# Performance work log

Hardware: AMD Instinct MI355X
Metric: run time of the kernel (lower is better)

## Reference

```python
import math
import jax, jax.numpy as jnp
import numpy as np

V, D, A, H, FF, L, MD = 500, 512, 512, 8, 2048, 6, 512
HD = A // H
B, S, T = 32, 512, 128


def setup_inputs() -> dict:
    key = jax.random.key(0)
    ks = jax.random.split(key, 40)
    init = lambda k, shape: (jax.random.normal(k, shape, jnp.float32) * 0.02)
    inp = {
        'memory': jax.random.normal(ks[0], (B, S, MD), jnp.float32),
        'memory_lens': jax.random.randint(ks[1], (B,), S // 2, S + 1),
        'ys_in_pad': jax.random.randint(ks[2], (B, T), 0, V),
        'ys_in_lens': jax.random.randint(ks[3], (B,), T // 2, T + 1),
        'emb': init(ks[4], (V, D)),
        'w_out': init(ks[5], (D, V)),
        'b_out': jnp.zeros((V,), jnp.float32),
        # per-layer params stacked on leading L axis (consumed by lax.scan)
        'ln_sa_g': jnp.ones((L, D), jnp.float32), 'ln_sa_b': jnp.zeros((L, D), jnp.float32),
        'sa_wq': init(ks[6], (L, D, A)), 'sa_bq': init(ks[7], (L, A)),
        'sa_wk': init(ks[8], (L, D, A)), 'sa_bk': init(ks[9], (L, A)),
        'sa_wv': init(ks[10], (L, D, A)), 'sa_bv': init(ks[11], (L, A)),
        'sa_wo': init(ks[12], (L, A, D)), 'sa_bo': init(ks[13], (L, D)),
        'ln_ca_g': jnp.ones((L, D), jnp.float32), 'ln_ca_b': jnp.zeros((L, D), jnp.float32),
        'ca_wq': init(ks[14], (L, D, A)), 'ca_bq': init(ks[15], (L, A)),
        'ca_wk': init(ks[16], (L, MD, A)), 'ca_bk': init(ks[17], (L, A)),
        'ca_wv': init(ks[18], (L, MD, A)), 'ca_bv': init(ks[19], (L, A)),
        'ca_wo': init(ks[20], (L, A, D)), 'ca_bo': init(ks[21], (L, D)),
        'ln_ff_g': jnp.ones((L, D), jnp.float32), 'ln_ff_b': jnp.zeros((L, D), jnp.float32),
        'ff_w1': init(ks[22], (L, D, FF)), 'ff_b1': init(ks[23], (L, FF)),
        'ff_w2': init(ks[24], (L, FF, D)), 'ff_b2': init(ks[25], (L, D)),
    }
    return inp


def _layernorm(x, g, b, eps=1e-5):
    m = jnp.mean(x, axis=-1, keepdims=True)
    v = jnp.mean(jnp.square(x - m), axis=-1, keepdims=True)
    return (x - m) * jax.lax.rsqrt(v + eps) * g + b


def _mha(q_in, k_in, v_in, mask, wq, bq, wk, bk, wv, bv, wo, bo):
    # mask: True = disallowed. (B, T, S) for self-attn, (B, 1, S) for cross-attn.
    b_, tq, _ = q_in.shape
    ts = k_in.shape[1]
    q = (q_in @ wq + bq).reshape(b_, tq, H, HD).transpose(0, 2, 1, 3)
    k = (k_in @ wk + bk).reshape(b_, ts, H, HD).transpose(0, 2, 1, 3)
    v = (v_in @ wv + bv).reshape(b_, ts, H, HD).transpose(0, 2, 1, 3)
    s = jnp.einsum('bhtd,bhsd->bhts', q, k) / math.sqrt(HD)
    # penalize_abs_values_gt(limit=50, penalty=1e-4) is identity in the forward
    # pass (it only injects an auxiliary gradient during training).
    s = jnp.where(mask[:, None, :, :], -jnp.inf, s)
    a = jax.nn.softmax(s, axis=-1)  # dropout p=0.0 in this config
    o = jnp.einsum('bhts,bhsd->bhtd', a, v).transpose(0, 2, 1, 3).reshape(b_, tq, A)
    return o @ wo + bo


def _forward(memory, memory_lens, ys_in_pad, ys_in_lens, emb, w_out, b_out, layer_params):
    t = ys_in_pad.shape[1]
    # make_pad_mask | ~subsequent_mask  -> (B, T, T), True = masked
    pad = jnp.arange(t)[None, :] >= ys_in_lens[:, None]            # (B, T)
    causal = ~jnp.tril(jnp.ones((t, t), bool))                     # (T, T)
    tgt_mask = pad[:, None, :] | causal[None]                      # (B, T, T)
    mem_mask = (jnp.arange(memory.shape[1])[None, :] >= memory_lens[:, None])[:, None, :]

    # embedding + sinusoidal positional encoding (dropout in eval = identity)
    pos = jnp.arange(t, dtype=jnp.float32)[:, None]
    div = jnp.exp(jnp.arange(0, D, 2, dtype=jnp.float32) * (-math.log(10000.0) / D))
    pe = jnp.zeros((t, D), jnp.float32)
    pe = pe.at[:, 0::2].set(jnp.sin(pos * div)).at[:, 1::2].set(jnp.cos(pos * div))
    x = emb[ys_in_pad] * math.sqrt(D) + pe[None]

    def step(tgt, p):
        tn = _layernorm(tgt, p['ln_sa_g'], p['ln_sa_b'])
        tgt = tgt + _mha(tn, tn, tn, tgt_mask,
                         p['sa_wq'], p['sa_bq'], p['sa_wk'], p['sa_bk'],
                         p['sa_wv'], p['sa_bv'], p['sa_wo'], p['sa_bo'])
        tn = _layernorm(tgt, p['ln_ca_g'], p['ln_ca_b'])
        tgt = tgt + _mha(tn, memory, memory, mem_mask,
                         p['ca_wq'], p['ca_bq'], p['ca_wk'], p['ca_bk'],
                         p['ca_wv'], p['ca_bv'], p['ca_wo'], p['ca_bo'])
        tn = _layernorm(tgt, p['ln_ff_g'], p['ln_ff_b'])
        h = tn @ p['ff_w1'] + p['ff_b1']
        h = h * jax.nn.sigmoid(h)  # Swish
        tgt = tgt + h @ p['ff_w2'] + p['ff_b2']
        return tgt, None

    x, _ = jax.lax.scan(step, x, layer_params)
    return x @ w_out + b_out  # (B, T, V) logits


_LAYER_KEYS = ['ln_sa_g', 'ln_sa_b', 'sa_wq', 'sa_bq', 'sa_wk', 'sa_bk', 'sa_wv', 'sa_bv',
               'sa_wo', 'sa_bo', 'ln_ca_g', 'ln_ca_b', 'ca_wq', 'ca_bq', 'ca_wk', 'ca_bk',
               'ca_wv', 'ca_bv', 'ca_wo', 'ca_bo', 'ln_ff_g', 'ln_ff_b',
               'ff_w1', 'ff_b1', 'ff_w2', 'ff_b2']


def reference(memory, memory_lens, ys_in_pad, ys_in_lens, emb, w_out, b_out,
              ln_sa_g, ln_sa_b, sa_wq, sa_bq, sa_wk, sa_bk, sa_wv, sa_bv, sa_wo, sa_bo,
              ln_ca_g, ln_ca_b, ca_wq, ca_bq, ca_wk, ca_bk, ca_wv, ca_bv, ca_wo, ca_bo,
              ln_ff_g, ln_ff_b, ff_w1, ff_b1, ff_w2, ff_b2):
    loc = locals()
    layer_params = {k: loc[k] for k in _LAYER_KEYS}
    return _forward(memory, memory_lens, ys_in_pad, ys_in_lens, emb, w_out, b_out, layer_params)
```

## Files before the change

### kernel.cpp

```cpp
#include <hip/hip_runtime.h>
#include <hip/hip_bf16.h>
#include <hip/hip_fp16.h>

constexpr int Bc = 32, Sc = 512, Tc = 128, Dc = 512, Ac = 512, Hc = 8;
constexpr int HDc = 64, FFc = 2048, Lc = 6, Vc = 500;
constexpr int NTOK = Bc * Tc;
constexpr int NMEM = Bc * Sc;

typedef unsigned short u16;
typedef __attribute__((ext_vector_type(8))) short short8;
typedef __attribute__((ext_vector_type(4))) float f32x4;

__device__ __forceinline__ u16 bfc(float x) {
  __hip_bfloat16 h = __float2bfloat16(x);
  return *reinterpret_cast<u16*>(&h);
}

__device__ __forceinline__ void gload16(const void* g, void* l) {
  __builtin_amdgcn_global_load_lds(
      (const __attribute__((address_space(1))) unsigned int*)g,
      (__attribute__((address_space(3))) unsigned int*)l, 16, 0, 0);
}

__device__ __forceinline__ float wave_sum(float v) {
#pragma unroll
  for (int o = 32; o > 0; o >>= 1) v += __shfl_down(v, o);
  return v;
}
__device__ __forceinline__ float wave_max(float v) {
#pragma unroll
  for (int o = 32; o > 0; o >>= 1) v = fmaxf(v, __shfl_down(v, o));
  return v;
}

__global__ __launch_bounds__(256) void embed_pe_k(const int* __restrict__ ys,
                                                  const float* __restrict__ emb,
                                                  float* __restrict__ x) {
  int tok = blockIdx.x;
  int t = tok & (Tc - 1);
  int id = ys[tok];
  int j = threadIdx.x;
  int d0 = 2 * j;
  const float cdiv = -9.210340371976184f / (float)Dc;
  float div = expf((float)d0 * cdiv);
  float ang = (float)t * div;
  float pe0 = sinf(ang), pe1 = cosf(ang);
  const float sc = 22.627416997969522f;
  long base = (long)tok * Dc + d0;
  long ebase = (long)id * Dc + d0;
  x[base]     = emb[ebase]     * sc + pe0;
  x[base + 1] = emb[ebase + 1] * sc + pe1;
}

__global__ __launch_bounds__(256) void layernorm_k(const float* __restrict__ x,
                                                   const float* __restrict__ g,
                                                   const float* __restrict__ bta,
                                                   u16* __restrict__ out) {
  int row = blockIdx.x;
  int tid = threadIdx.x;
  const float* xr = x + (long)row * Dc;
  float2 xv = *(const float2*)(xr + tid * 2);
  __shared__ float red[4];
  float s = wave_sum(xv.x + xv.y);
  if ((tid & 63) == 0) red[tid >> 6] = s;
  __syncthreads();
  float mean = (red[0] + red[1] + red[2] + red[3]) * (1.0f / Dc);
  float dx0 = xv.x - mean, dx1 = xv.y - mean;
  __syncthreads();
  float s2 = wave_sum(dx0 * dx0 + dx1 * dx1);
  if ((tid & 63) == 0) red[tid >> 6] = s2;
  __syncthreads();
  float var = (red[0] + red[1] + red[2] + red[3]) * (1.0f / Dc);
  float rstd = rsqrtf(var + 1e-5f);
  ushort2 o;
  o.x = bfc(dx0 * rstd * g[2 * tid] + bta[2 * tid]);
  o.y = bfc(dx1 * rstd * g[2 * tid + 1] + bta[2 * tid + 1]);
  *(ushort2*)(out + (long)row * Dc + tid * 2) = o;
}

__global__ __launch_bounds__(256) void wtrans_k(const float* __restrict__ src,
                                                u16* __restrict__ dst,
                                                int K, int N, long srcStride, long dstStride) {
  int z = blockIdx.z;
  src += z * srcStride;
  dst += z * dstStride;
  __shared__ float t[32][33];
  int n0 = blockIdx.x * 32, k0 = blockIdx.y * 32;
  int tx = threadIdx.x & 31, ty = threadIdx.x >> 5;
#pragma unroll
  for (int i = 0; i < 4; i++) {
    int n = n0 + tx;
    t[ty + 8 * i][tx] = (n < N) ? src[(long)(k0 + ty + 8 * i) * N + n] : 0.0f;
  }
  __syncthreads();
#pragma unroll
  for (int i = 0; i < 4; i++) {
    dst[(long)(n0 + ty + 8 * i) * K + k0 + tx] = bfc(t[tx][ty + 8 * i]);
  }
}

__global__ __launch_bounds__(256) void vtrans_k(const u16* __restrict__ V,
                                                u16* __restrict__ Vt, int Scur) {
  int b = blockIdx.z;
  int c0 = blockIdx.x * 32, s0 = blockIdx.y * 32;
  __shared__ u16 t[32][33];
  int tx = threadIdx.x & 31, ty = threadIdx.x >> 5;
#pragma unroll
  for (int i = 0; i < 4; i++)
    t[ty + 8 * i][tx] = V[((long)b * Scur + s0 + ty + 8 * i) * 512 + c0 + tx];
  __syncthreads();
#pragma unroll
  for (int i = 0; i < 4; i++)
    Vt[((long)b * 512 + c0 + ty + 8 * i) * Scur + s0 + tx] = t[tx][ty + 8 * i];
}

__global__ __launch_bounds__(256) void f2b_k(const float* __restrict__ in,
                                             u16* __restrict__ out, long n) {
  long i = ((long)blockIdx.x * 256 + threadIdx.x) * 4;
  if (i >= n) return;
  float4 v = *(const float4*)(in + i);
  ushort4 o;
  o.x = bfc(v.x); o.y = bfc(v.y); o.z = bfc(v.z); o.w = bfc(v.w);
  *(ushort4*)(out + i) = o;
}

template <int BMW, int OMODE, bool BIAS, bool RES, bool SWISH, bool NCH>
__global__ __launch_bounds__(256) void mgemm_k(
    const u16* __restrict__ A, const u16* __restrict__ Bt,
    const float* __restrict__ bias0, const float* __restrict__ bias1,
    const float* __restrict__ bias2,
    void* __restrict__ Cv, const float* __restrict__ R,
    int N, int K, int lda, int ldb, int ldc, int nbi,
    long batAo, long batAi, long batBo, long batBi, long batCo, long batCi) {
  constexpr int BM = BMW * 32;
  int z = blockIdx.z;
  int bo = z / nbi, bi = z - bo * nbi;
  const u16* Ab = A + bo * batAo + bi * batAi;
  const u16* Bb = Bt + bo * batBo + bi * batBi;
  long coff = bo * batCo + bi * batCi;
  const float* bias = nullptr;
  if constexpr (BIAS) bias = (bi == 0) ? bias0 : ((bi == 1) ? bias1 : bias2);
  int m0 = blockIdx.y * BM, n0 = blockIdx.x * 128;

  __shared__ __align__(16) u16 As[BM * 32];
  __shared__ __align__(16) u16 Bs[128 * 32];

  int tid = threadIdx.x;
  int lane = tid & 63, wid = tid >> 6;
  int wm = wid >> 1, wn = wid & 1;
  int fr = lane & 15, grp = lane >> 4;

  f32x4 acc[BMW][4];
#pragma unroll
  for (int i = 0; i < BMW; i++)
#pragma unroll
    for (int j = 0; j < 4; j++) acc[i][j] = (f32x4){0.f, 0.f, 0.f, 0.f};

  const u16* ga = Ab + (long)(m0 + (tid >> 2)) * lda + ((tid & 3) << 3);
  const u16* gb = Bb + (long)(n0 + (tid >> 2)) * ldb + ((tid & 3) << 3);
  u16* lA = &As[tid * 8];
  u16* lB = &Bs[tid * 8];

  for (int kt = 0; kt < K; kt += 32) {
    gload16(ga + kt, lA);
    if constexpr (BM == 128) gload16(ga + kt + (long)64 * lda, lA + 2048);
    gload16(gb + kt, lB);
    gload16(gb + kt + (long)64 * ldb, lB + 2048);
    __syncthreads();
    short8 av[BMW], bv[4];
#pragma unroll
    for (int i = 0; i < BMW; i++)
      av[i] = *(const short8*)&As[(wm * BMW * 16 + i * 16 + fr) * 32 + grp * 8];
#pragma unroll
    for (int j = 0; j < 4; j++)
      bv[j] = *(const short8*)&Bs[(wn * 64 + j * 16 + fr) * 32 + grp * 8];
#pragma unroll
    for (int i = 0; i < BMW; i++)
#pragma unroll
      for (int j = 0; j < 4; j++)
        acc[i][j] = __builtin_amdgcn_mfma_f32_16x16x32_bf16(av[i], bv[j], acc[i][j], 0, 0, 0);
    __syncthreads();
  }

  int rbase = m0 + wm * BMW * 16 + grp * 4;
  int cbase = n0 + wn * 64 + fr;
#pragma unroll
  for (int i = 0; i < BMW; i++) {
#pragma unroll
    for (int j = 0; j < 4; j++) {
      int col = cbase + j * 16;
      if (NCH && col >= N) continue;
      float bb = 0.0f;
      if constexpr (BIAS) bb = bias[col];
#pragma unroll
      for (int r = 0; r < 4; r++) {
        int row = rbase + i * 16 + r;
        float v = acc[i][j][r] + bb;
        long idx = coff + (long)row * ldc + col;
        if constexpr (RES) v += R[idx];
        if constexpr (SWISH) v = v / (1.0f + expf(-v));
        if constexpr (OMODE == 0) ((u16*)Cv)[idx] = bfc(v);
        else ((float*)Cv)[idx] = v;
      }
    }
  }
}

template <int SKV, int KVBLK, bool CAUSAL>
__global__ __launch_bounds__(256) void fattn_k(
    const u16* __restrict__ Q, const u16* __restrict__ Kg, const u16* __restrict__ Vtg,
    u16* __restrict__ O, const int* __restrict__ lens) {
  constexpr int NJ  = KVBLK / 16;
  constexpr int NKV = KVBLK / 32;
  constexpr int NT  = SKV / KVBLK;
  constexpr int KST = 72;
  constexpr int VST = KVBLK + 8;
  constexpr int CHK = KVBLK * 8 / 256;
  constexpr int CHV = 64 * (KVBLK / 8) / 256;

  __shared__ __align__(16) u16 Ks[KVBLK * KST];
  __shared__ __align__(16) u16 Vs[64 * VST];
  __shared__ __align__(16) u16 Ps[128 * VST];

  int bh = blockIdx.x; int b = bh >> 3, h = bh & 7;
  int tid = threadIdx.x, lane = tid & 63, wid = tid >> 6;
  int fr = lane & 15, grp = lane >> 4;
  int len = lens[b];

  short8 qa[2][2];
  {
    const u16* qp = Q + ((long)b * Tc + wid * 32 + fr) * 512 + h * 64 + grp * 8;
#pragma unroll
    for (int i = 0; i < 2; i++)
#pragma unroll
      for (int k2 = 0; k2 < 2; k2++)
        qa[i][k2] = *(const short8*)(qp + (long)i * 16 * 512 + k2 * 32);
  }

  float m_run[2][4], l_run[2][4];
  f32x4 acc_o[2][4];
#pragma unroll
  for (int i = 0; i < 2; i++)
#pragma unroll
    for (int r = 0; r < 4; r++) { m_run[i][r] = -1e30f; l_run[i][r] = 0.0f; }
#pragma unroll
  for (int i = 0; i < 2; i++)
#pragma unroll
    for (int j = 0; j < 4; j++) acc_o[i][j] = (f32x4){0.f, 0.f, 0.f, 0.f};

  const u16* Kbase = Kg + ((long)b * SKV) * 512 + h * 64;
  const u16* Vbase = Vtg + ((long)b * 512 + h * 64) * SKV;

  short8 kreg[CHK], vreg[CHV];
#pragma unroll
  for (int c = 0; c < CHK; c++) {
    int idx = tid + 256 * c; int kv = idx >> 3, s = idx & 7;
    kreg[c] = *(const short8*)(Kbase + (long)kv * 512 + s * 8);
  }
#pragma unroll
  for (int c = 0; c < CHV; c++) {
    int idx = tid + 256 * c; int d = idx / (KVBLK / 8), sk = idx % (KVBLK / 8);
    vreg[c] = *(const short8*)(Vbase + (long)d * SKV + sk * 8);
  }

  for (int t = 0; t < NT; t++) {
    int kv0 = t * KVBLK;
    __syncthreads();
#pragma unroll
    for (int c = 0; c < CHK; c++) {
      int idx = tid + 256 * c; int kv = idx >> 3, s = idx & 7;
      *(short8*)&Ks[kv * KST + s * 8] = kreg[c];
    }
#pragma unroll
    for (int c = 0; c < CHV; c++) {
      int idx = tid + 256 * c; int d = idx / (KVBLK / 8), sk = idx % (KVBLK / 8);
      *(short8*)&Vs[d * VST + sk * 8] = vreg[c];
    }
    __syncthreads();
    if (t + 1 < NT) {
      int kvn = kv0 + KVBLK;
#pragma unroll
      for (int c = 0; c < CHK; c++) {
        int idx = tid + 256 * c; int kv = idx >> 3, s = idx & 7;
        kreg[c] = *(const short8*)(Kbase + (long)(kvn + kv) * 512 + s * 8);
      }
#pragma unroll
      for (int c = 0; c < CHV; c++) {
        int idx = tid + 256 * c; int d = idx / (KVBLK / 8), sk = idx % (KVBLK / 8);
        vreg[c] = *(const short8*)(Vbase + (long)d * SKV + kvn + sk * 8);
      }
    }

    int jmax = NJ;
    if constexpr (CAUSAL) jmax = (wid * 32 + 31 - kv0) / 16 + 1;

    f32x4 accs[2][NJ];
#pragma unroll
    for (int j = 0; j < NJ; j++) {
      if (CAUSAL && j >= jmax) continue;
      short8 bv0 = *(const short8*)&Ks[(j * 16 + fr) * KST + grp * 8];
      short8 bv1 = *(const short8*)&Ks[(j * 16 + fr) * KST + 32 + grp * 8];
#pragma unroll
      for (int i = 0; i < 2; i++) {
        f32x4 a = __builtin_amdgcn_mfma_f32_16x16x32_bf16(qa[i][0], bv0, (f32x4){0.f,0.f,0.f,0.f}, 0, 0, 0);
        accs[i][j] = __builtin_amdgcn_mfma_f32_16x16x32_bf16(qa[i][1], bv1, a, 0, 0, 0);
      }
    }

    float alpha[2][4];
#pragma unroll
    for (int i = 0; i < 2; i++) {
#pragma unroll
      for (int r = 0; r < 4; r++) {
        int qrow = wid * 32 + i * 16 + grp * 4 + r;
        float vmax = -1e30f;
#pragma unroll
        for (int j = 0; j < NJ; j++) {
          if (CAUSAL && j >= jmax) continue;
          int kvb = kv0 + j * 16 + fr;
          float s = accs[i][j][r] * 0.125f;
          bool msk = (kvb >= len) || (CAUSAL && kvb > qrow);
          s = msk ? -1e30f : s;
          accs[i][j][r] = s;
          vmax = fmaxf(vmax, s);
        }
        vmax = fmaxf(vmax, __shfl_xor(vmax, 1));
        vmax = fmaxf(vmax, __shfl_xor(vmax, 2));
        vmax = fmaxf(vmax, __shfl_xor(vmax, 4));
        vmax = fmaxf(vmax, __shfl_xor(vmax, 8));
        float mn = fmaxf(m_run[i][r], vmax);
        float al = __expf(m_run[i][r] - mn);
        m_run[i][r] = mn;
        alpha[i][r] = al;
        float rs = 0.0f;
#pragma unroll
        for (int j = 0; j < NJ; j++) {
          if (CAUSAL && j >= jmax) continue;
          float p = __expf(accs[i][j][r] - mn);
          accs[i][j][r] = p;
          rs += p;
        }
        rs += __shfl_xor(rs, 1);
        rs += __shfl_xor(rs, 2);
        rs += __shfl_xor(rs, 4);
        rs += __shfl_xor(rs, 8);
        l_run[i][r] = l_run[i][r] * al + rs;
      }
    }

#pragma unroll
    for (int i = 0; i < 2; i++)
#pragma unroll
      for (int j = 0; j < NJ; j++) {
        if (CAUSAL && j >= jmax) continue;
#pragma unroll
        for (int r = 0; r < 4; r++) {
          int prow = wid * 32 + i * 16 + grp * 4 + r;
          Ps[prow * VST + j * 16 + fr] = bfc(accs[i][j][r]);
        }
      }

#pragma unroll
    for (int i = 0; i < 2; i++)
#pragma unroll
      for (int jd = 0; jd < 4; jd++)
#pragma unroll
        for (int r = 0; r < 4; r++)
          acc_o[i][jd][r] *= alpha[i][r];

    int kvmax = NKV;
    if constexpr (CAUSAL) kvmax = wid + 1;
#pragma unroll
    for (int kk = 0; kk < NKV; kk++) {
      if (CAUSAL && kk >= kvmax) continue;
      short8 pa[2];
#pragma unroll
      for (int i = 0; i < 2; i++)
        pa[i] = *(const short8*)&Ps[(wid * 32 + i * 16 + fr) * VST + kk * 32 + grp * 8];
#pragma unroll
      for (int jd = 0; jd < 4; jd++) {
        short8 vb = *(const short8*)&Vs[(jd * 16 + fr) * VST + kk * 32 + grp * 8];
#pragma unroll
        for (int i = 0; i < 2; i++)
          acc_o[i][jd] = __builtin_amdgcn_mfma_f32_16x16x32_bf16(pa[i], vb, acc_o[i][jd], 0, 0, 0);
      }
    }
  }

#pragma unroll
  for (int i = 0; i < 2; i++) {
#pragma unroll
    for (int r = 0; r < 4; r++) {
      float inv = 1.0f / l_run[i][r];
      long tok = (long)b * Tc + wid * 32 + i * 16 + grp * 4 + r;
#pragma unroll
      for (int jd = 0; jd < 4; jd++)
        O[tok * 512 + h * 64 + jd * 16 + fr] = bfc(acc_o[i][jd][r] * inv);
    }
  }
}

extern "C" void kernel_launch(void* const* d_in, const int* in_sizes, int n_in,
                              void* d_out, int out_size, void* d_ws, size_t ws_size,
                              hipStream_t stream) {
  const float* memory   = (const float*)d_in[0];
  const int*   mem_lens = (const int*)d_in[1];
  const int*   ys       = (const int*)d_in[2];
  const int*   ys_lens  = (const int*)d_in[3];
  const float* emb      = (const float*)d_in[4];
  const float* w_out    = (const float*)d_in[5];
  const float* b_out    = (const float*)d_in[6];
  const float* pp[26];
  for (int i = 0; i < 26; i++) pp[i] = (const float*)d_in[7 + i];

  constexpr long PLW = 4194304;
  constexpr long OFF_SAQ = 0, OFF_SAK = 262144, OFF_SAV = 524288, OFF_SAO = 786432,
                 OFF_CAQ = 1048576, OFF_CAK = 1310720, OFF_CAV = 1572864,
                 OFF_CAO = 1835008, OFF_FF1 = 2097152, OFF_FF2 = 3145728,
                 OFF_WOUT = 6 * PLW;
  u16*   Wt   = (u16*)d_ws;
  float* X    = (float*)(Wt + 25427968);
  u16*   TO   = (u16*)(X + 2097152);
  u16*   QKV  = TO + 2097152;
  u16*   memb = QKV + 3 * 2097152;
  u16*   Kb   = memb + 8388608;
  u16*   SCw  = Kb + 8388608;
  u16*   Vt   = SCw + 16777216;
  float* OUT  = (float*)d_out;

  auto WT = [&](const float* src, long dstoff, int K, int N, int Npad, int Lz,
                long srcStride, long dstStride) {
    dim3 g(Npad / 32, K / 32, Lz);
    wtrans_k<<<g, 256, 0, stream>>>(src, Wt + dstoff, K, N, srcStride, dstStride);
  };
  WT(pp[2],  OFF_SAQ, 512, 512, 512, Lc, 262144, PLW);
  WT(pp[4],  OFF_SAK, 512, 512, 512, Lc, 262144, PLW);
  WT(pp[6],  OFF_SAV, 512, 512, 512, Lc, 262144, PLW);
  WT(pp[8],  OFF_SAO, 512, 512, 512, Lc, 262144, PLW);
  WT(pp[12], OFF_CAQ, 512, 512, 512, Lc, 262144, PLW);
  WT(pp[14], OFF_CAK, 512, 512, 512, Lc, 262144, PLW);
  WT(pp[16], OFF_CAV, 512, 512, 512, Lc, 262144, PLW);
  WT(pp[18], OFF_CAO, 512, 512, 512, Lc, 262144, PLW);
  WT(pp[22], OFF_FF1, 512, 2048, 2048, Lc, 1048576, PLW);
  WT(pp[24], OFF_FF2, 2048, 512, 512, Lc, 1048576, PLW);
  WT(w_out,  OFF_WOUT, 512, 500, 512, 1, 0, 0);

  f2b_k<<<(NMEM * Dc / 4 + 255) / 256, 256, 0, stream>>>(memory, memb, (long)NMEM * Dc);
  embed_pe_k<<<NTOK, 256, 0, stream>>>(ys, emb, X);

  for (int l = 0; l < Lc; l++) {
    const u16* WtL = Wt + (long)l * PLW;

    layernorm_k<<<NTOK, 256, 0, stream>>>(X, pp[0] + (long)l * Dc, pp[1] + (long)l * Dc, TO);
    mgemm_k<2, 0, true, false, false, false><<<dim3(4, 64, 3), 256, 0, stream>>>(
        TO, WtL + OFF_SAQ, pp[3] + (long)l * Ac, pp[5] + (long)l * Ac, pp[7] + (long)l * Ac,
        QKV, nullptr, 512, 512, 512, 512, 512, 3, 0, 0, 0, 262144, 0, 2097152);
    vtrans_k<<<dim3(16, 4, Bc), 256, 0, stream>>>(QKV + 2 * 2097152, Vt, Tc);
    fattn_k<128, 128, true><<<256, 256, 0, stream>>>(
        QKV, QKV + 2097152, Vt, TO, ys_lens);
    mgemm_k<2, 1, true, true, false, false><<<dim3(4, 64, 1), 256, 0, stream>>>(
        TO, WtL + OFF_SAO, pp[9] + (long)l * Dc, nullptr, nullptr, X, X,
        512, 512, 512, 512, 512, 1, 0, 0, 0, 0, 0, 0);

    layernorm_k<<<NTOK, 256, 0, stream>>>(X, pp[10] + (long)l * Dc, pp[11] + (long)l * Dc, TO);
    mgemm_k<2, 0, true, false, false, false><<<dim3(4, 64, 1), 256, 0, stream>>>(
        TO, WtL + OFF_CAQ, pp[13] + (long)l * Ac, nullptr, nullptr, QKV, nullptr,
        512, 512, 512, 512, 512, 1, 0, 0, 0, 0, 0, 0);
    mgemm_k<4, 0, true, false, false, false><<<dim3(4, 128, 2), 256, 0, stream>>>(
        memb, WtL + OFF_CAK, pp[15] + (long)l * Ac, pp[17] + (long)l * Ac, nullptr,
        Kb, nullptr, 512, 512, 512, 512, 512, 2, 0, 0, 0, 262144, 0, 8388608);
    vtrans_k<<<dim3(16, 16, Bc), 256, 0, stream>>>(SCw, Vt, Sc);
    fattn_k<512, 64, false><<<256, 256, 0, stream>>>(
        QKV, Kb, Vt, TO, mem_lens);
    mgemm_k<2, 1, true, true, false, false><<<dim3(4, 64, 1), 256, 0, stream>>>(
        TO, WtL + OFF_CAO, pp[19] + (long)l * Dc, nullptr, nullptr, X, X,
        512, 512, 512, 512, 512, 1, 0, 0, 0, 0, 0, 0);

    layernorm_k<<<NTOK, 256, 0, stream>>>(X, pp[20] + (long)l * Dc, pp[21] + (long)l * Dc, TO);
    mgemm_k<2, 0, true, false, true, false><<<dim3(16, 64, 1), 256, 0, stream>>>(
        TO, WtL + OFF_FF1, pp[23] + (long)l * FFc, nullptr, nullptr, SCw, nullptr,
        2048, 512, 512, 512, 2048, 1, 0, 0, 0, 0, 0, 0);
    mgemm_k<2, 1, true, true, false, false><<<dim3(4, 64, 1), 256, 0, stream>>>(
        SCw, WtL + OFF_FF2, pp[25] + (long)l * Dc, nullptr, nullptr, X, X,
        512, 2048, 2048, 2048, 512, 1, 0, 0, 0, 0, 0, 0);
  }

  f2b_k<<<(NTOK * Dc / 4 + 255) / 256, 256, 0, stream>>>(X, TO, (long)NTOK * Dc);
  mgemm_k<2, 1, true, false, false, true><<<dim3(4, 64, 1), 256, 0, stream>>>(
      TO, Wt + OFF_WOUT, b_out, nullptr, nullptr, OUT, nullptr,
      500, 512, 512, 512, 500, 1, 0, 0, 0, 0, 0, 0);
}
```

Baseline: 1.305 ms.

## Double-buffer GEMM LDS, drop V transpose, add attention row-split and tile skipping

The GEMM kernel now double-buffers its shared-memory tiles so the next K-slice loads while the current one is multiplied. The separate V-transpose kernels are removed, and the attention kernel transposes V into shared memory itself with scalar stores. It also skips KV tiles past the causal limit or the sequence length, and splits query rows across blocks for cross-attention. Larger BM tiles are used for the QKV and FF1 GEMMs. The scalar transposed LDS stores may cause bank conflicts, and doubling LDS can reduce occupancy.

```diff
diff --git a/kernel.cpp b/kernel.cpp
--- a/kernel.cpp
+++ b/kernel.cpp
@@ -99,21 +99,6 @@
   }
 }
 
-__global__ __launch_bounds__(256) void vtrans_k(const u16* __restrict__ V,
-                                                u16* __restrict__ Vt, int Scur) {
-  int b = blockIdx.z;
-  int c0 = blockIdx.x * 32, s0 = blockIdx.y * 32;
-  __shared__ u16 t[32][33];
-  int tx = threadIdx.x & 31, ty = threadIdx.x >> 5;
-#pragma unroll
-  for (int i = 0; i < 4; i++)
-    t[ty + 8 * i][tx] = V[((long)b * Scur + s0 + ty + 8 * i) * 512 + c0 + tx];
-  __syncthreads();
-#pragma unroll
-  for (int i = 0; i < 4; i++)
-    Vt[((long)b * 512 + c0 + ty + 8 * i) * Scur + s0 + tx] = t[tx][ty + 8 * i];
-}
-
 __global__ __launch_bounds__(256) void f2b_k(const float* __restrict__ in,
                                              u16* __restrict__ out, long n) {
   long i = ((long)blockIdx.x * 256 + threadIdx.x) * 4;
@@ -142,8 +127,8 @@
   if constexpr (BIAS) bias = (bi == 0) ? bias0 : ((bi == 1) ? bias1 : bias2);
   int m0 = blockIdx.y * BM, n0 = blockIdx.x * 128;
 
-  __shared__ __align__(16) u16 As[BM * 32];
-  __shared__ __align__(16) u16 Bs[128 * 32];
+  __shared__ __align__(16) u16 As[2][BM * 32];
+  __shared__ __align__(16) u16 Bs[2][128 * 32];
 
   int tid = threadIdx.x;
   int lane = tid & 63, wid = tid >> 6;
@@ -158,29 +143,41 @@
 
   const u16* ga = Ab + (long)(m0 + (tid >> 2)) * lda + ((tid & 3) << 3);
   const u16* gb = Bb + (long)(n0 + (tid >> 2)) * ldb + ((tid & 3) << 3);
-  u16* lA = &As[tid * 8];
-  u16* lB = &Bs[tid * 8];
-
-  for (int kt = 0; kt < K; kt += 32) {
+
+  auto STAGE = [&](int buf, int kt) {
+    u16* lA = &As[buf][tid * 8];
+    u16* lB = &Bs[buf][tid * 8];
     gload16(ga + kt, lA);
     if constexpr (BM == 128) gload16(ga + kt + (long)64 * lda, lA + 2048);
     gload16(gb + kt, lB);
     gload16(gb + kt + (long)64 * ldb, lB + 2048);
-    __syncthreads();
+  };
+
+  auto COMPUTE = [&](int buf) {
     short8 av[BMW], bv[4];
 #pragma unroll
     for (int i = 0; i < BMW; i++)
-      av[i] = *(const short8*)&As[(wm * BMW * 16 + i * 16 + fr) * 32 + grp * 8];
+      av[i] = *(const short8*)&As[buf][(wm * BMW * 16 + i * 16 + fr) * 32 + grp * 8];
 #pragma unroll
     for (int j = 0; j < 4; j++)
-      bv[j] = *(const short8*)&Bs[(wn * 64 + j * 16 + fr) * 32 + grp * 8];
+      bv[j] = *(const short8*)&Bs[buf][(wn * 64 + j * 16 + fr) * 32 + grp * 8];
 #pragma unroll
     for (int i = 0; i < BMW; i++)
 #pragma unroll
       for (int j = 0; j < 4; j++)
         acc[i][j] = __builtin_amdgcn_mfma_f32_16x16x32_bf16(av[i], bv[j], acc[i][j], 0, 0, 0);
+  };
+
+  STAGE(0, 0);
+  __syncthreads();
+  int cur = 0;
+  for (int kt = 32; kt < K; kt += 32) {
+    STAGE(cur ^ 1, kt);
+    COMPUTE(cur);
     __syncthreads();
-  }
+    cur ^= 1;
+  }
+  COMPUTE(cur);
 
   int rbase = m0 + wm * BMW * 16 + grp * 4;
   int cbase = n0 + wn * 64 + fr;
@@ -206,113 +203,114 @@
   }
 }
 
-template <int SKV, int KVBLK, bool CAUSAL>
+template <int SKV, int KVBLK, bool CAUSAL, int IQ>
 __global__ __launch_bounds__(256) void fattn_k(
-    const u16* __restrict__ Q, const u16* __restrict__ Kg, const u16* __restrict__ Vtg,
+    const u16* __restrict__ Q, const u16* __restrict__ Kg, const u16* __restrict__ Vg,
     u16* __restrict__ O, const int* __restrict__ lens) {
   constexpr int NJ  = KVBLK / 16;
   constexpr int NKV = KVBLK / 32;
   constexpr int NT  = SKV / KVBLK;
   constexpr int KST = 72;
   constexpr int VST = KVBLK + 8;
-  constexpr int CHK = KVBLK * 8 / 256;
-  constexpr int CHV = 64 * (KVBLK / 8) / 256;
+  constexpr int WR  = 16 * IQ;
+  constexpr int WGR = 64 * IQ;
+  constexpr int CH  = KVBLK / 32;
 
   __shared__ __align__(16) u16 Ks[KVBLK * KST];
   __shared__ __align__(16) u16 Vs[64 * VST];
-  __shared__ __align__(16) u16 Ps[128 * VST];
+  __shared__ __align__(16) u16 Ps[WGR * VST];
 
   int bh = blockIdx.x; int b = bh >> 3, h = bh & 7;
+  int row00 = blockIdx.y * WGR;
   int tid = threadIdx.x, lane = tid & 63, wid = tid >> 6;
   int fr = lane & 15, grp = lane >> 4;
   int len = lens[b];
-
-  short8 qa[2][2];
+  int row0w = row00 + wid * WR;
+
+  short8 qa[IQ][2];
   {
-    const u16* qp = Q + ((long)b * Tc + wid * 32 + fr) * 512 + h * 64 + grp * 8;
-#pragma unroll
-    for (int i = 0; i < 2; i++)
+    const u16* qp = Q + ((long)b * Tc + row0w + fr) * 512 + h * 64 + grp * 8;
+#pragma unroll
+    for (int i = 0; i < IQ; i++)
 #pragma unroll
       for (int k2 = 0; k2 < 2; k2++)
         qa[i][k2] = *(const short8*)(qp + (long)i * 16 * 512 + k2 * 32);
   }
 
-  float m_run[2][4], l_run[2][4];
-  f32x4 acc_o[2][4];
-#pragma unroll
-  for (int i = 0; i < 2; i++)
+  float m_run[IQ][4], l_run[IQ][4];
+  f32x4 acc_o[IQ][4];
+#pragma unroll
+  for (int i = 0; i < IQ; i++)
 #pragma unroll
     for (int r = 0; r < 4; r++) { m_run[i][r] = -1e30f; l_run[i][r] = 0.0f; }
 #pragma unroll
-  for (int i = 0; i < 2; i++)
+  for (int i = 0; i < IQ; i++)
 #pragma unroll
     for (int j = 0; j < 4; j++) acc_o[i][j] = (f32x4){0.f, 0.f, 0.f, 0.f};
 
   const u16* Kbase = Kg + ((long)b * SKV) * 512 + h * 64;
-  const u16* Vbase = Vtg + ((long)b * 512 + h * 64) * SKV;
-
-  short8 kreg[CHK], vreg[CHV];
-#pragma unroll
-  for (int c = 0; c < CHK; c++) {
+  const u16* Vbase = Vg + ((long)b * SKV) * 512 + h * 64;
+
+  int NTeff = NT;
+  if constexpr (CAUSAL) NTeff = (row00 + WGR - 1) / KVBLK + 1;
+  int lenT = (len + KVBLK - 1) / KVBLK;
+  if (lenT < NTeff) NTeff = lenT;
+
+  short8 kreg[CH], vreg[CH];
+#pragma unroll
+  for (int c = 0; c < CH; c++) {
     int idx = tid + 256 * c; int kv = idx >> 3, s = idx & 7;
     kreg[c] = *(const short8*)(Kbase + (long)kv * 512 + s * 8);
-  }
-#pragma unroll
-  for (int c = 0; c < CHV; c++) {
-    int idx = tid + 256 * c; int d = idx / (KVBLK / 8), sk = idx % (KVBLK / 8);
-    vreg[c] = *(const short8*)(Vbase + (long)d * SKV + sk * 8);
-  }
-
-  for (int t = 0; t < NT; t++) {
+    vreg[c] = *(const short8*)(Vbase + (long)kv * 512 + s * 8);
+  }
+
+  for (int t = 0; t < NTeff; t++) {
     int kv0 = t * KVBLK;
     __syncthreads();
 #pragma unroll
-    for (int c = 0; c < CHK; c++) {
+    for (int c = 0; c < CH; c++) {
       int idx = tid + 256 * c; int kv = idx >> 3, s = idx & 7;
       *(short8*)&Ks[kv * KST + s * 8] = kreg[c];
-    }
-#pragma unroll
-    for (int c = 0; c < CHV; c++) {
-      int idx = tid + 256 * c; int d = idx / (KVBLK / 8), sk = idx % (KVBLK / 8);
-      *(short8*)&Vs[d * VST + sk * 8] = vreg[c];
+#pragma unroll
+      for (int j = 0; j < 8; j++)
+        Vs[(s * 8 + j) * VST + kv] = (u16)vreg[c][j];
     }
     __syncthreads();
-    if (t + 1 < NT) {
+    if (t + 1 < NTeff) {
       int kvn = kv0 + KVBLK;
 #pragma unroll
-      for (int c = 0; c < CHK; c++) {
+      for (int c = 0; c < CH; c++) {
         int idx = tid + 256 * c; int kv = idx >> 3, s = idx & 7;
         kreg[c] = *(const short8*)(Kbase + (long)(kvn + kv) * 512 + s * 8);
-      }
-#pragma unroll
-      for (int c = 0; c < CHV; c++) {
-        int idx = tid + 256 * c; int d = idx / (KVBLK / 8), sk = idx % (KVBLK / 8);
-        vreg[c] = *(const short8*)(Vbase + (long)d * SKV + kvn + sk * 8);
+        vreg[c] = *(const short8*)(Vbase + (long)(kvn + kv) * 512 + s * 8);
       }
     }
 
     int jmax = NJ;
-    if constexpr (CAUSAL) jmax = (wid * 32 + 31 - kv0) / 16 + 1;
-
-    f32x4 accs[2][NJ];
+    if constexpr (CAUSAL) {
+      jmax = (row0w + WR - 1 - kv0) / 16 + 1;
+      if (jmax > NJ) jmax = NJ;
+    }
+
+    f32x4 accs[IQ][NJ];
 #pragma unroll
     for (int j = 0; j < NJ; j++) {
       if (CAUSAL && j >= jmax) continue;
       short8 bv0 = *(const short8*)&Ks[(j * 16 + fr) * KST + grp * 8];
       short8 bv1 = *(const short8*)&Ks[(j * 16 + fr) * KST + 32 + grp * 8];
 #pragma unroll
-      for (int i = 0; i < 2; i++) {
+      for (int i = 0; i < IQ; i++) {
         f32x4 a = __builtin_amdgcn_mfma_f32_16x16x32_bf16(qa[i][0], bv0, (f32x4){0.f,0.f,0.f,0.f}, 0, 0, 0);
         accs[i][j] = __builtin_amdgcn_mfma_f32_16x16x32_bf16(qa[i][1], bv1, a, 0, 0, 0);
       }
     }
 
-    float alpha[2][4];
-#pragma unroll
-    for (int i = 0; i < 2; i++) {
+    float alpha[IQ][4];
+#pragma unroll
+    for (int i = 0; i < IQ; i++) {
 #pragma unroll
       for (int r = 0; r < 4; r++) {
-        int qrow = wid * 32 + i * 16 + grp * 4 + r;
+        int qrow = row0w + i * 16 + grp * 4 + r;
         float vmax = -1e30f;
 #pragma unroll
         for (int j = 0; j < NJ; j++) {
@@ -349,19 +347,19 @@
     }
 
 #pragma unroll
-    for (int i = 0; i < 2; i++)
+    for (int i = 0; i < IQ; i++)
 #pragma unroll
       for (int j = 0; j < NJ; j++) {
         if (CAUSAL && j >= jmax) continue;
 #pragma unroll
         for (int r = 0; r < 4; r++) {
-          int prow = wid * 32 + i * 16 + grp * 4 + r;
+          int prow = wid * WR + i * 16 + grp * 4 + r;
           Ps[prow * VST + j * 16 + fr] = bfc(accs[i][j][r]);
         }
       }
 
 #pragma unroll
-    for (int i = 0; i < 2; i++)
+    for (int i = 0; i < IQ; i++)
 #pragma unroll
       for (int jd = 0; jd < 4; jd++)
 #pragma unroll
@@ -369,30 +367,33 @@
           acc_o[i][jd][r] *= alpha[i][r];
 
     int kvmax = NKV;
-    if constexpr (CAUSAL) kvmax = wid + 1;
+    if constexpr (CAUSAL) {
+      kvmax = (row0w + WR - 1 - kv0) / 32 + 1;
+      if (kvmax > NKV) kvmax = NKV;
+    }
 #pragma unroll
     for (int kk = 0; kk < NKV; kk++) {
       if (CAUSAL && kk >= kvmax) continue;
-      short8 pa[2];
-#pragma unroll
-      for (int i = 0; i < 2; i++)
-        pa[i] = *(const short8*)&Ps[(wid * 32 + i * 16 + fr) * VST + kk * 32 + grp * 8];
+      short8 pa[IQ];
+#pragma unroll
+      for (int i = 0; i < IQ; i++)
+        pa[i] = *(const short8*)&Ps[(wid * WR + i * 16 + fr) * VST + kk * 32 + grp * 8];
 #pragma unroll
       for (int jd = 0; jd < 4; jd++) {
         short8 vb = *(const short8*)&Vs[(jd * 16 + fr) * VST + kk * 32 + grp * 8];
 #pragma unroll
-        for (int i = 0; i < 2; i++)
+        for (int i = 0; i < IQ; i++)
           acc_o[i][jd] = __builtin_amdgcn_mfma_f32_16x16x32_bf16(pa[i], vb, acc_o[i][jd], 0, 0, 0);
       }
     }
   }
 
 #pragma unroll
-  for (int i = 0; i < 2; i++) {
+  for (int i = 0; i < IQ; i++) {
 #pragma unroll
     for (int r = 0; r < 4; r++) {
       float inv = 1.0f / l_run[i][r];
-      long tok = (long)b * Tc + wid * 32 + i * 16 + grp * 4 + r;
+      long tok = (long)b * Tc + row0w + i * 16 + grp * 4 + r;
 #pragma unroll
       for (int jd = 0; jd < 4; jd++)
         O[tok * 512 + h * 64 + jd * 16 + fr] = bfc(acc_o[i][jd][r] * inv);
@@ -424,8 +425,7 @@
   u16*   QKV  = TO + 2097152;
   u16*   memb = QKV + 3 * 2097152;
   u16*   Kb   = memb + 8388608;
-  u16*   SCw  = Kb + 8388608;
-  u16*   Vt   = SCw + 16777216;
+  u16*   SCR  = Kb + 8388608;
   float* OUT  = (float*)d_out;
 
   auto WT = [&](const float* src, long dstoff, int K, int N, int Npad, int Lz,
@@ -452,12 +452,11 @@
     const u16* WtL = Wt + (long)l * PLW;
 
     layernorm_k<<<NTOK, 256, 0, stream>>>(X, pp[0] + (long)l * Dc, pp[1] + (long)l * Dc, TO);
-    mgemm_k<2, 0, true, false, false, false><<<dim3(4, 64, 3), 256, 0, stream>>>(
+    mgemm_k<4, 0, true, false, false, false><<<dim3(4, 32, 3), 256, 0, stream>>>(
         TO, WtL + OFF_SAQ, pp[3] + (long)l * Ac, pp[5] + (long)l * Ac, pp[7] + (long)l * Ac,
         QKV, nullptr, 512, 512, 512, 512, 512, 3, 0, 0, 0, 262144, 0, 2097152);
-    vtrans_k<<<dim3(16, 4, Bc), 256, 0, stream>>>(QKV + 2 * 2097152, Vt, Tc);
-    fattn_k<128, 128, true><<<256, 256, 0, stream>>>(
-        QKV, QKV + 2097152, Vt, TO, ys_lens);
+    fattn_k<128, 128, true, 2><<<dim3(256, 1), 256, 0, stream>>>(
+        QKV, QKV + 2097152, QKV + 2 * 2097152, TO, ys_lens);
     mgemm_k<2, 1, true, true, false, false><<<dim3(4, 64, 1), 256, 0, stream>>>(
         TO, WtL + OFF_SAO, pp[9] + (long)l * Dc, nullptr, nullptr, X, X,
         512, 512, 512, 512, 512, 1, 0, 0, 0, 0, 0, 0);
@@ -469,19 +468,18 @@
     mgemm_k<4, 0, true, false, false, false><<<dim3(4, 128, 2), 256, 0, stream>>>(
         memb, WtL + OFF_CAK, pp[15] + (long)l * Ac, pp[17] + (long)l * Ac, nullptr,
         Kb, nullptr, 512, 512, 512, 512, 512, 2, 0, 0, 0, 262144, 0, 8388608);
-    vtrans_k<<<dim3(16, 16, Bc), 256, 0, stream>>>(SCw, Vt, Sc);
-    fattn_k<512, 64, false><<<256, 256, 0, stream>>>(
-        QKV, Kb, Vt, TO, mem_lens);
+    fattn_k<512, 64, false, 1><<<dim3(256, 2), 256, 0, stream>>>(
+        QKV, Kb, SCR, TO, mem_lens);
     mgemm_k<2, 1, true, true, false, false><<<dim3(4, 64, 1), 256, 0, stream>>>(
         TO, WtL + OFF_CAO, pp[19] + (long)l * Dc, nullptr, nullptr, X, X,
         512, 512, 512, 512, 512, 1, 0, 0, 0, 0, 0, 0);
 
     layernorm_k<<<NTOK, 256, 0, stream>>>(X, pp[20] + (long)l * Dc, pp[21] + (long)l * Dc, TO);
-    mgemm_k<2, 0, true, false, true, false><<<dim3(16, 64, 1), 256, 0, stream>>>(
-        TO, WtL + OFF_FF1, pp[23] + (long)l * FFc, nullptr, nullptr, SCw, nullptr,
+    mgemm_k<4, 0, true, false, true, false><<<dim3(16, 32, 1), 256, 0, stream>>>(
+        TO, WtL + OFF_FF1, pp[23] + (long)l * FFc, nullptr, nullptr, SCR, nullptr,
         2048, 512, 512, 512, 2048, 1, 0, 0, 0, 0, 0, 0);
     mgemm_k<2, 1, true, true, false, false><<<dim3(4, 64, 1), 256, 0, stream>>>(
-        SCw, WtL + OFF_FF2, pp[25] + (long)l * Dc, nullptr, nullptr, X, X,
+        SCR, WtL + OFF_FF2, pp[25] + (long)l * Dc, nullptr, nullptr, X, X,
         512, 2048, 2048, 2048, 512, 1, 0, 0, 0, 0, 0, 0);
   }
 
```

Result: faster. 1.252 ms (-4.1%).
